# Optimization experiments

Hardware: AMD Instinct MI355X
Metric: run time of the kernel (lower is better)

The kernel has to match this reference:

```python
import jax, jax.numpy as jnp
import numpy as np

B, T, C = 4, 2048, 1024   # batch, seq_len, n_embd
H, D = 16, 64             # num heads, head dim (H*D == C)


def setup_inputs() -> dict:
    key = jax.random.key(0)
    ks = jax.random.split(key, 6)
    scale = 0.02
    x = jax.random.normal(ks[0], (B, T, C), dtype=jnp.float32)
    Wq = jax.random.normal(ks[1], (H, C, D), dtype=jnp.float32) * scale
    Wk = jax.random.normal(ks[2], (H, C, D), dtype=jnp.float32) * scale
    Wv = jax.random.normal(ks[3], (H, C, D), dtype=jnp.float32) * scale
    Wp = jax.random.normal(ks[4], (C, C), dtype=jnp.float32) * scale
    bp = jnp.zeros((C,), dtype=jnp.float32)
    return {"x": x, "Wq": Wq, "Wk": Wk, "Wv": Wv, "Wp": Wp, "bp": bp}


def reference(x, Wq, Wk, Wv, Wp, bp):
    # Batched per-head projections (equivalent to the per-head nn.Linear loop)
    q = jnp.einsum('btc,hcd->bhtd', x, Wq)
    k = jnp.einsum('btc,hcd->bhtd', x, Wk)
    v = jnp.einsum('btc,hcd->bhtd', x, Wv)
    # NOTE: original code scales by C**-0.5 where C = n_embd (not head dim)
    scores = jnp.einsum('bhtd,bhsd->bhts', q, k) * (C ** -0.5)
    causal = jnp.tril(jnp.ones((T, T), dtype=bool))  # [T, T]
    scores = jnp.where(causal, scores, -jnp.inf)
    att = jax.nn.softmax(scores, axis=-1)            # [B, H, T, T]
    out = jnp.einsum('bhts,bhsd->bhtd', att, v)      # [B, H, T, D]
    # concat heads (order matches torch.cat over head list) then output proj
    out = out.transpose(0, 2, 1, 3).reshape(B, T, H * D)
    return out @ Wp + bp
```

## Files before the change

### kernel.cpp

```cpp
#include <hip/hip_runtime.h>
#include <hip/hip_bf16.h>


#define B_ 4
#define T_ 2048
#define C_ 1024
#define H_ 16
#define D_ 64
#define M_ (B_*T_)

typedef unsigned short u16;
typedef unsigned short ushort8 __attribute__((ext_vector_type(8)));
typedef unsigned int uint4v __attribute__((ext_vector_type(4)));
typedef int int2v __attribute__((ext_vector_type(2)));
typedef __attribute__((ext_vector_type(8))) short bf16x8;
typedef __attribute__((ext_vector_type(4))) float f32x4;
typedef __attribute__((ext_vector_type(16))) float f32x16;

__device__ __forceinline__ u16 f2bf(float f) {
    __hip_bfloat16 h = __float2bfloat16(f);
    return *reinterpret_cast<u16*>(&h);
}

__device__ __forceinline__ unsigned pkt(float lo, float hi2) {
    return __builtin_amdgcn_perm(__float_as_uint(hi2), __float_as_uint(lo), 0x07060302u);
}

__device__ __forceinline__ void gload_lds16(const void* g, void* lds) {
    __builtin_amdgcn_global_load_lds((const __attribute__((address_space(1))) unsigned int*)g,
                                     (__attribute__((address_space(3))) unsigned int*)lds, 16, 0, 0);
}

__global__ __launch_bounds__(256) void cast_x(const float* __restrict__ in, u16* __restrict__ out) {
    int i = (blockIdx.x * 256 + threadIdx.x) * 8;
    float4 a = *reinterpret_cast<const float4*>(in + i);
    float4 b = *reinterpret_cast<const float4*>(in + i + 4);
    ushort8 o;
    o[0]=f2bf(a.x); o[1]=f2bf(a.y); o[2]=f2bf(a.z); o[3]=f2bf(a.w);
    o[4]=f2bf(b.x); o[5]=f2bf(b.y); o[6]=f2bf(b.z); o[7]=f2bf(b.w);
    *reinterpret_cast<ushort8*>(out + i) = o;
}

__device__ __forceinline__ void ttile64(const float* __restrict__ in, int ldin,
                                        u16* __restrict__ out, int ldout, float scale) {
    __shared__ float t[64][65];
    const int tid = threadIdx.x;
    {
        int c = tid & 63, rr = tid >> 6;
        #pragma unroll
        for (int i = 0; i < 16; ++i) {
            int r = i * 4 + rr;
            t[r][c] = in[(size_t)r * ldin + c];
        }
    }
    __syncthreads();
    {
        int r2 = tid & 63, cg = tid >> 6;
        #pragma unroll
        for (int i = 0; i < 16; ++i) {
            int cc = i * 4 + cg;
            out[(size_t)cc * ldout + r2] = f2bf(t[r2][cc] * scale);
        }
    }
}

__global__ __launch_bounds__(256) void tw_qkv(const float* __restrict__ Wq, const float* __restrict__ Wk,
                                              const float* __restrict__ Wv, u16* __restrict__ Wt) {
    const int z = blockIdx.y;
    const int which = z >> 4, h = z & 15;
    const float* W = (which == 0 ? Wq : which == 1 ? Wk : Wv) + (size_t)h * C_ * D_;
    const int r0 = blockIdx.x * 64;
    const float scale = (which == 0) ? 0.03125f * 1.4426950408889634f : 1.f;
    ttile64(W + (size_t)r0 * D_, D_, Wt + (size_t)(which * 16 + h) * 64 * C_ + r0, C_, scale);
}

__global__ __launch_bounds__(256) void tw_p(const float* __restrict__ Wp, u16* __restrict__ Wpt) {
    const int r0 = blockIdx.x * 64, c0 = blockIdx.y * 64;
    ttile64(Wp + (size_t)r0 * C_ + c0, C_, Wpt + (size_t)c0 * C_ + r0, C_, 1.f);
}

__global__ __launch_bounds__(256) void tv(const u16* __restrict__ v, u16* __restrict__ vT) {
    __shared__ u16 t[64][72];
    const int tid = threadIdx.x;
    const int t0 = blockIdx.x * 64, bh = blockIdx.y;
    const u16* src = v + ((size_t)bh * T_ + t0) * D_;
    #pragma unroll
    for (int it = 0; it < 2; ++it) {
        int idx = it * 256 + tid;
        int r = idx >> 3, c8 = (idx & 7) * 8;
        *reinterpret_cast<ushort8*>(&t[r][c8]) =
            *reinterpret_cast<const ushort8*>(src + (size_t)r * D_ + c8);
    }
    __syncthreads();
    #pragma unroll
    for (int it = 0; it < 2; ++it) {
        int idx = it * 256 + tid;
        int d = idx >> 3, c8 = (idx & 7) * 8;
        ushort8 w;
        #pragma unroll
        for (int i = 0; i < 8; ++i) w[i] = t[c8 + i][d];
        *reinterpret_cast<ushort8*>(vT + ((size_t)bh * D_ + d) * T_ + t0 + c8) = w;
    }
}

__device__ __forceinline__ void gemm128_core(const u16* __restrict__ A, const u16* __restrict__ Bt,
                                             int m0, int n0, int K,
                                             u16* Asm, u16* Bsm, f32x4 (&acc)[4][4]) {
    const int tid = threadIdx.x;
    const int wid = tid >> 6, lane = tid & 63;
    const int l16 = lane & 15, lq = lane >> 4;
    const int wm = wid >> 1, wn = wid & 1;
    const int srow = lane >> 2;
    const int scol = (lane & 3) * 8;

    for (int k0 = 0; k0 < K; k0 += 32) {
        __syncthreads();
        #pragma unroll
        for (int it = 0; it < 2; ++it) {
            int row = wid * 32 + it * 16 + srow;
            gload_lds16(A  + (size_t)(m0 + row) * K + k0 + scol, Asm + wid * 1024 + it * 512);
            gload_lds16(Bt + (size_t)(n0 + row) * K + k0 + scol, Bsm + wid * 1024 + it * 512);
        }
        __syncthreads();
        bf16x8 af[4], bfr[4];
        #pragma unroll
        for (int t = 0; t < 4; ++t) {
            af[t]  = *reinterpret_cast<const bf16x8*>(Asm + (wm * 64 + t * 16 + l16) * 32 + lq * 8);
            bfr[t] = *reinterpret_cast<const bf16x8*>(Bsm + (wn * 64 + t * 16 + l16) * 32 + lq * 8);
        }
        #pragma unroll
        for (int mt = 0; mt < 4; ++mt)
            #pragma unroll
            for (int nt = 0; nt < 4; ++nt)
                acc[mt][nt] = __builtin_amdgcn_mfma_f32_16x16x32_bf16(af[mt], bfr[nt], acc[mt][nt], 0, 0, 0);
    }
}

__global__ __launch_bounds__(256) void qkv_gemm(const u16* __restrict__ xb, const u16* __restrict__ Wt,
                                                u16* __restrict__ q, u16* __restrict__ k, u16* __restrict__ v) {
    __shared__ u16 Asm[128 * 32], Bsm[128 * 32];
    f32x4 acc[4][4];
    #pragma unroll
    for (int i = 0; i < 4; ++i)
        #pragma unroll
        for (int j = 0; j < 4; ++j) { acc[i][j][0]=0.f; acc[i][j][1]=0.f; acc[i][j][2]=0.f; acc[i][j][3]=0.f; }
    const int m0 = blockIdx.x * 128, n0 = blockIdx.y * 128;
    gemm128_core(xb, Wt, m0, n0, C_, Asm, Bsm, acc);

    const int tid = threadIdx.x, wid = tid >> 6, lane = tid & 63;
    const int l16 = lane & 15, lq = lane >> 4;
    const int wm = wid >> 1, wn = wid & 1;
    #pragma unroll
    for (int mt = 0; mt < 4; ++mt) {
        #pragma unroll
        for (int j = 0; j < 4; ++j) {
            int m = m0 + wm * 64 + mt * 16 + lq * 4 + j;
            int b = m >> 11, t = m & (T_ - 1);
            #pragma unroll
            for (int nt = 0; nt < 4; ++nt) {
                int n = n0 + wn * 64 + nt * 16 + l16;
                int which = n >> 10, h = (n >> 6) & 15, d = n & 63;
                u16* dst = (which == 0 ? q : which == 1 ? k : v);
                dst[((size_t)(b * H_ + h) * T_ + t) * D_ + d] = f2bf(acc[mt][nt][j]);
            }
        }
    }
}

__global__ __launch_bounds__(256) void out_gemm(const u16* __restrict__ ob, const u16* __restrict__ Wpt,
                                                const float* __restrict__ bp, float* __restrict__ out) {
    __shared__ u16 Asm[128 * 32], Bsm[128 * 32];
    f32x4 acc[4][4];
    #pragma unroll
    for (int i = 0; i < 4; ++i)
        #pragma unroll
        for (int j = 0; j < 4; ++j) { acc[i][j][0]=0.f; acc[i][j][1]=0.f; acc[i][j][2]=0.f; acc[i][j][3]=0.f; }
    const int m0 = blockIdx.x * 128, n0 = blockIdx.y * 128;
    gemm128_core(ob, Wpt, m0, n0, C_, Asm, Bsm, acc);

    const int tid = threadIdx.x, wid = tid >> 6, lane = tid & 63;
    const int l16 = lane & 15, lq = lane >> 4;
    const int wm = wid >> 1, wn = wid & 1;
    #pragma unroll
    for (int mt = 0; mt < 4; ++mt) {
        #pragma unroll
        for (int j = 0; j < 4; ++j) {
            int m = m0 + wm * 64 + mt * 16 + lq * 4 + j;
            #pragma unroll
            for (int nt = 0; nt < 4; ++nt) {
                int n = n0 + wn * 64 + nt * 16 + l16;
                out[(size_t)m * C_ + n] = acc[mt][nt][j] + bp[n];
            }
        }
    }
}

template<int CUR>
__device__ __forceinline__ void attn_tile(const char* const (&pf)[4], const bf16x8 (&qf)[4],
                                          const f32x16& z16, float& lrun,
                                          f32x16& oacc0, f32x16& oacc1,
                                          bool isdiag, int relq, int hi) {
    f32x16 st0, st1;
    __builtin_amdgcn_s_setprio(1);
    {
        bf16x8 ka0 = *reinterpret_cast<const bf16x8*>(pf[0] + CUR * 8192);
        bf16x8 ka1 = *reinterpret_cast<const bf16x8*>(pf[0] + CUR * 8192 + 4096);
        st0 = __builtin_amdgcn_mfma_f32_32x32x16_bf16(ka0, qf[0], z16, 0, 0, 0);
        st1 = __builtin_amdgcn_mfma_f32_32x32x16_bf16(ka1, qf[0], z16, 0, 0, 0);
    }
    #pragma unroll
    for (int kc = 1; kc < 4; ++kc) {
        bf16x8 ka0 = *reinterpret_cast<const bf16x8*>(pf[kc] + CUR * 8192);
        bf16x8 ka1 = *reinterpret_cast<const bf16x8*>(pf[kc] + CUR * 8192 + 4096);
        st0 = __builtin_amdgcn_mfma_f32_32x32x16_bf16(ka0, qf[kc], st0, 0, 0, 0);
        st1 = __builtin_amdgcn_mfma_f32_32x32x16_bf16(ka1, qf[kc], st1, 0, 0, 0);
    }
    __builtin_amdgcn_s_setprio(0);

    if (isdiag) {
        #pragma unroll
        for (int rr = 0; rr < 16; ++rr) {
            int sl = (rr & 3) + 8 * (rr >> 2) + 4 * hi;
            if (sl > relq)      st0[rr] = -INFINITY;
            if (sl + 32 > relq) st1[rr] = -INFINITY;
        }
    }

    float rsum = 0.f;
    #pragma unroll
    for (int rr = 0; rr < 16; ++rr) {
        st0[rr] = __builtin_amdgcn_exp2f(st0[rr]);
        st1[rr] = __builtin_amdgcn_exp2f(st1[rr]);
        rsum += st0[rr] + st1[rr];
    }
    rsum += __shfl_xor(rsum, 32);
    lrun += rsum;

    bf16x8 pa0, pa1, pa2, pa3;
#if __has_builtin(__builtin_amdgcn_permlane32_swap)
#define MK_PA(PA, SV, RB)                                                          \
    {                                                                              \
        int X0 = (int)pkt(SV[RB + 0], SV[RB + 1]);                                 \
        int X1 = (int)pkt(SV[RB + 2], SV[RB + 3]);                                 \
        int Y0 = (int)pkt(SV[RB + 4], SV[RB + 5]);                                 \
        int Y1 = (int)pkt(SV[RB + 6], SV[RB + 7]);                                 \
        int2v r0 = __builtin_amdgcn_permlane32_swap(X0, Y0, false, false);         \
        int2v r1 = __builtin_amdgcn_permlane32_swap(X1, Y1, false, false);         \
        uint4v w; w[0] = (unsigned)r0[0]; w[1] = (unsigned)r1[0];                  \
        w[2] = (unsigned)r0[1]; w[3] = (unsigned)r1[1];                            \
        PA = __builtin_bit_cast(bf16x8, w);                                        \
    }
#else
#define MK_PA(PA, SV, RB)                                                          \
    {                                                                              \
        unsigned X0 = pkt(SV[RB + 0], SV[RB + 1]);                                 \
        unsigned X1 = pkt(SV[RB + 2], SV[RB + 3]);                                 \
        unsigned Y0 = pkt(SV[RB + 4], SV[RB + 5]);                                 \
        unsigned sX0 = __shfl_xor(X0, 32), sY0 = __shfl_xor(Y0, 32);               \
        unsigned Y1 = pkt(SV[RB + 6], SV[RB + 7]);                                 \
        unsigned sX1 = __shfl_xor(X1, 32), sY1 = __shfl_xor(Y1, 32);               \
        uint4v w;                                                                  \
        w[0] = hi ? sY0 : X0; w[1] = hi ? sY1 : X1;                                \
        w[2] = hi ? Y0 : sX0; w[3] = hi ? Y1 : sX1;                                \
        PA = __builtin_bit_cast(bf16x8, w);                                        \
    }
#endif
    MK_PA(pa0, st0, 0); MK_PA(pa1, st0, 8); MK_PA(pa2, st1, 0); MK_PA(pa3, st1, 8);
#undef MK_PA

    __builtin_amdgcn_s_setprio(1);
#define PV_STEP(SCJ, PAV)                                                          \
    {                                                                              \
        bf16x8 va0 = *reinterpret_cast<const bf16x8*>(pf[SCJ] + 16384 + CUR * 8192);        \
        bf16x8 va1 = *reinterpret_cast<const bf16x8*>(pf[SCJ] + 16384 + CUR * 8192 + 4096); \
        oacc0 = __builtin_amdgcn_mfma_f32_32x32x16_bf16(va0, PAV, oacc0, 0, 0, 0); \
        oacc1 = __builtin_amdgcn_mfma_f32_32x32x16_bf16(va1, PAV, oacc1, 0, 0, 0); \
    }
    PV_STEP(0, pa0) PV_STEP(1, pa1) PV_STEP(2, pa2) PV_STEP(3, pa3)
#undef PV_STEP
    __builtin_amdgcn_s_setprio(0);
}

__global__ __launch_bounds__(256) void attn_mfma(const u16* __restrict__ q,
                                                 const u16* __restrict__ k,
                                                 const u16* __restrict__ vT,
                                                 u16* __restrict__ o) {
    __shared__ u16 smem[2][2][4096];

    const int tid  = threadIdx.x;
    const int wid  = tid >> 6;
    const int lane = tid & 63;
    const int l31  = lane & 31;
    const int hi   = lane >> 5;

    const int lin = blockIdx.x;
    const int r   = lin & 255;
    const int f   = lin >> 8;
    const int e   = r & 7;
    int qb, bh;
    if      (f == 0) { qb = e;      bh = (r >> 3);      }
    else if (f == 1) { qb = 15 - e; bh = (r >> 3);      }
    else if (f == 2) { qb = e + 8;  bh = (r >> 3) + 32; }
    else             { qb = 7 - e;  bh = (r >> 3) + 32; }

    const int q0 = qb * 128;
    const size_t base = (size_t)bh * T_ * D_;
    const u16* kp  = k  + base;
    const u16* vtp = vT + (size_t)bh * D_ * T_;
    const int qglob = q0 + wid * 32 + l31;

    bf16x8 qf[4];
    {
        const u16* qp = q + base + (size_t)qglob * D_;
        #pragma unroll
        for (int kc = 0; kc < 4; ++kc)
            qf[kc] = *reinterpret_cast<const bf16x8*>(qp + kc * 16 + hi * 8);
    }

    const int rw0 = wid * 8 + (lane >> 3);
    const int rw1 = rw0 + 32;
    const int cg  = (lane & 7) ^ (rw0 & 7);
    const u16* gK0 = kp + rw0 * D_ + cg * 8;
    const u16* gK1 = kp + rw1 * D_ + cg * 8;
    const u16* gV0 = vtp + (size_t)rw0 * T_ + cg * 8;
    const u16* gV1 = vtp + (size_t)rw1 * T_ + cg * 8;

    u16* sbase = &smem[0][0][0];
    u16* dK0 = sbase + wid * 512;
    u16* dK1 = sbase + 2048 + wid * 512;
    u16* dV0 = sbase + 8192 + wid * 512;
    u16* dV1 = sbase + 8192 + 2048 + wid * 512;

    const char* pf[4];
    #pragma unroll
    for (int j = 0; j < 4; ++j)
        pf[j] = reinterpret_cast<const char*>(sbase) + l31 * 128 + (((j * 2 + hi) ^ (l31 & 7)) << 4);

    float lrun = 0.f;
    f32x16 oacc0, oacc1, z16;
    #pragma unroll
    for (int rr = 0; rr < 16; ++rr) { oacc0[rr] = 0.f; oacc1[rr] = 0.f; z16[rr] = 0.f; }

    const int ntile  = 2 * qb + 2;
    const int diag_t = 2 * qb + (wid >> 1);
    const int relq   = 32 * (wid & 1) + l31;

#define STG(BUFOFF)                                                                \
    {                                                                              \
        gload_lds16(gK0, dK0 + (BUFOFF)); gload_lds16(gK1, dK1 + (BUFOFF));        \
        gload_lds16(gV0, dV0 + (BUFOFF)); gload_lds16(gV1, dV1 + (BUFOFF));        \
        gK0 += 64 * D_; gK1 += 64 * D_; gV0 += 64; gV1 += 64;                      \
    }

    STG(0);
    __syncthreads();

    for (int tt = 0; tt < ntile; tt += 2) {
        if (tt + 1 < ntile) STG(4096);
        if (tt <= diag_t)
            attn_tile<0>(pf, qf, z16, lrun, oacc0, oacc1, tt == diag_t, relq, hi);
        __syncthreads();
        if (tt + 2 < ntile) STG(0);
        if (tt + 1 <= diag_t)
            attn_tile<1>(pf, qf, z16, lrun, oacc0, oacc1, tt + 1 == diag_t, relq, hi);
        __syncthreads();
    }
#undef STG

    float linv = 1.f / lrun;
    float* ot = reinterpret_cast<float*>(sbase) + wid * 2048;
    #pragma unroll
    for (int rr = 0; rr < 16; ++rr) {
        int d0v = (rr & 3) + 8 * (rr >> 2) + 4 * hi;
        int d1v = d0v + 32;
        ot[l31 * 64 + (((d0v >> 2) ^ (l31 & 7)) << 2) + (d0v & 3)] = oacc0[rr] * linv;
        ot[l31 * 64 + (((d1v >> 2) ^ (l31 & 7)) << 2) + (d1v & 3)] = oacc1[rr] * linv;
    }

    const int b = bh >> 4, h = bh & 15;
    const int qrow = lane >> 1;
    const int d0 = (lane & 1) * 32;
    u16 tmp[32];
    #pragma unroll
    for (int i = 0; i < 8; ++i) {
        int g = ((d0 >> 2) + i) ^ (qrow & 7);
        float4 fv = *reinterpret_cast<const float4*>(&ot[qrow * 64 + (g << 2)]);
        tmp[i * 4 + 0] = f2bf(fv.x); tmp[i * 4 + 1] = f2bf(fv.y);
        tmp[i * 4 + 2] = f2bf(fv.z); tmp[i * 4 + 3] = f2bf(fv.w);
    }
    u16* orow = o + ((size_t)b * T_ + q0 + wid * 32 + qrow) * C_ + h * 64 + d0;
    #pragma unroll
    for (int j = 0; j < 4; ++j)
        *reinterpret_cast<ushort8*>(orow + j * 8) = *reinterpret_cast<ushort8*>(&tmp[j * 8]);
}

extern "C" void kernel_launch(void* const* d_in, const int* in_sizes, int n_in,
                              void* d_out, int out_size, void* d_ws, size_t ws_size,
                              hipStream_t stream) {
    const float* x  = (const float*)d_in[0];
    const float* Wq = (const float*)d_in[1];
    const float* Wk = (const float*)d_in[2];
    const float* Wv = (const float*)d_in[3];
    const float* Wp = (const float*)d_in[4];
    const float* bp = (const float*)d_in[5];
    float* out = (float*)d_out;

    const size_t E = (size_t)M_ * C_;
    u16* xb  = (u16*)d_ws;
    u16* qb  = xb  + E;
    u16* kb  = qb  + E;
    u16* vb  = kb  + E;
    u16* obf = vb  + E;
    u16* Wt  = obf + E;
    u16* Wpt = Wt  + (size_t)3072 * 1024;
    u16* vTb = xb;

    cast_x<<<(E / 2048), 256, 0, stream>>>(x, xb);
    tw_qkv<<<dim3(16, 48), 256, 0, stream>>>(Wq, Wk, Wv, Wt);
    tw_p<<<dim3(16, 16), 256, 0, stream>>>(Wp, Wpt);

    qkv_gemm<<<dim3(M_ / 128, 3072 / 128), 256, 0, stream>>>(xb, Wt, qb, kb, vb);

    tv<<<dim3(T_ / 64, B_ * H_), 256, 0, stream>>>(vb, vTb);

    attn_mfma<<<dim3(1024), 256, 0, stream>>>(qb, kb, vTb, obf);

    out_gemm<<<dim3(M_ / 128, C_ / 128), 256, 0, stream>>>(obf, Wpt, bp, out);
}
```

Measured before the change: 165.4 us.

## Rewrite projection GEMMs with 256x128 tiles, triple-buffered LDS and swizzle

Replaces the 128x128, K=32 single-buffered GEMM core with a 256x128 tile, 512-thread kernel that uses K=64 stages in a three-deep LDS ring buffer with explicit vmcnt waits, so global-to-LDS loads overlap MFMA work. LDS rows are XOR-swizzled to avoid bank conflicts, and each wave computes a 128x32 sub-tile. The aim is to remove load stalls and per-step barrier overhead in the QKV and output projections. In exchange it uses much more LDS per block (144KB) and more registers, which limits occupancy and halves the number of blocks.

```diff
diff --git a/kernel.cpp b/kernel.cpp
--- a/kernel.cpp
+++ b/kernel.cpp
@@ -103,62 +103,108 @@
     }
 }
 
-__device__ __forceinline__ void gemm128_core(const u16* __restrict__ A, const u16* __restrict__ Bt,
-                                             int m0, int n0, int K,
-                                             u16* Asm, u16* Bsm, f32x4 (&acc)[4][4]) {
+__device__ __forceinline__ void gemm256_core(const u16* __restrict__ A, const u16* __restrict__ Bt,
+                                             int m0, int n0, u16* lds, f32x4 (&acc)[8][2]) {
     const int tid = threadIdx.x;
     const int wid = tid >> 6, lane = tid & 63;
     const int l16 = lane & 15, lq = lane >> 4;
-    const int wm = wid >> 1, wn = wid & 1;
-    const int srow = lane >> 2;
-    const int scol = (lane & 3) * 8;
-
-    for (int k0 = 0; k0 < K; k0 += 32) {
-        __syncthreads();
-        #pragma unroll
-        for (int it = 0; it < 2; ++it) {
-            int row = wid * 32 + it * 16 + srow;
-            gload_lds16(A  + (size_t)(m0 + row) * K + k0 + scol, Asm + wid * 1024 + it * 512);
-            gload_lds16(Bt + (size_t)(n0 + row) * K + k0 + scol, Bsm + wid * 1024 + it * 512);
-        }
-        __syncthreads();
-        bf16x8 af[4], bfr[4];
-        #pragma unroll
-        for (int t = 0; t < 4; ++t) {
-            af[t]  = *reinterpret_cast<const bf16x8*>(Asm + (wm * 64 + t * 16 + l16) * 32 + lq * 8);
-            bfr[t] = *reinterpret_cast<const bf16x8*>(Bsm + (wn * 64 + t * 16 + l16) * 32 + lq * 8);
-        }
-        #pragma unroll
-        for (int mt = 0; mt < 4; ++mt)
+    const int wr = wid >> 2, wc = wid & 3;
+
+    const u16* sA[4];
+    const u16* sB[2];
+    #pragma unroll
+    for (int it = 0; it < 4; ++it) {
+        int slot = it * 512 + tid, row = slot >> 3, gd = slot & 7;
+        sA[it] = A + (size_t)(m0 + row) * C_ + ((gd ^ (row & 7)) * 8);
+    }
+    #pragma unroll
+    for (int it = 0; it < 2; ++it) {
+        int slot = it * 512 + tid, row = slot >> 3, gd = slot & 7;
+        sB[it] = Bt + (size_t)(n0 + row) * C_ + ((gd ^ (row & 7)) * 8);
+    }
+    const int dA = wid * 512 + lane * 8;
+    const int dB = 16384 + wid * 512 + lane * 8;
+
+    const char* lb = reinterpret_cast<const char*>(lds);
+    const int arow = wr * 128 + l16;
+    const int brow = wc * 32 + l16;
+    const int g0 = (lq ^ (l16 & 7)) * 16;
+    const int g1 = ((4 + lq) ^ (l16 & 7)) * 16;
+    const int aoff0 = arow * 128 + g0, aoff1 = arow * 128 + g1;
+    const int boff0 = 32768 + brow * 128 + g0, boff1 = 32768 + brow * 128 + g1;
+
+#define STAGE6(BUFU16)                                                              \
+    {                                                                               \
+        _Pragma("unroll")                                                           \
+        for (int it = 0; it < 4; ++it) {                                            \
+            gload_lds16(sA[it], lds + (BUFU16) + it * 4096 + dA);                   \
+            sA[it] += 64;                                                           \
+        }                                                                           \
+        _Pragma("unroll")                                                           \
+        for (int it = 0; it < 2; ++it) {                                            \
+            gload_lds16(sB[it], lds + (BUFU16) + it * 4096 + dB);                   \
+            sB[it] += 64;                                                           \
+        }                                                                           \
+    }
+
+    STAGE6(0);
+    STAGE6(24576);
+
+    #pragma unroll
+    for (int t = 0; t < 16; ++t) {
+        if (t + 2 < 16) STAGE6(((t + 2) % 3) * 24576);
+        if (t + 2 < 16)      { asm volatile("s_waitcnt vmcnt(12)" ::: "memory"); }
+        else if (t + 1 < 16) { asm volatile("s_waitcnt vmcnt(6)" ::: "memory"); }
+        else                 { asm volatile("s_waitcnt vmcnt(0)" ::: "memory"); }
+        __builtin_amdgcn_sched_barrier(0);
+        __builtin_amdgcn_s_barrier();
+        __builtin_amdgcn_sched_barrier(0);
+
+        const char* lbuf = lb + (size_t)((t % 3) * 24576) * 2;
+        __builtin_amdgcn_s_setprio(1);
+        #pragma unroll
+        for (int kc = 0; kc < 2; ++kc) {
+            bf16x8 bf0 = *reinterpret_cast<const bf16x8*>(lbuf + (kc ? boff1 : boff0));
+            bf16x8 bf1 = *reinterpret_cast<const bf16x8*>(lbuf + (kc ? boff1 : boff0) + 2048);
             #pragma unroll
-            for (int nt = 0; nt < 4; ++nt)
-                acc[mt][nt] = __builtin_amdgcn_mfma_f32_16x16x32_bf16(af[mt], bfr[nt], acc[mt][nt], 0, 0, 0);
-    }
-}
-
-__global__ __launch_bounds__(256) void qkv_gemm(const u16* __restrict__ xb, const u16* __restrict__ Wt,
-                                                u16* __restrict__ q, u16* __restrict__ k, u16* __restrict__ v) {
-    __shared__ u16 Asm[128 * 32], Bsm[128 * 32];
-    f32x4 acc[4][4];
-    #pragma unroll
-    for (int i = 0; i < 4; ++i)
-        #pragma unroll
-        for (int j = 0; j < 4; ++j) { acc[i][j][0]=0.f; acc[i][j][1]=0.f; acc[i][j][2]=0.f; acc[i][j][3]=0.f; }
-    const int m0 = blockIdx.x * 128, n0 = blockIdx.y * 128;
-    gemm128_core(xb, Wt, m0, n0, C_, Asm, Bsm, acc);
+            for (int mt = 0; mt < 8; ++mt) {
+                bf16x8 af = *reinterpret_cast<const bf16x8*>(lbuf + (kc ? aoff1 : aoff0) + mt * 2048);
+                acc[mt][0] = __builtin_amdgcn_mfma_f32_16x16x32_bf16(af, bf0, acc[mt][0], 0, 0, 0);
+                acc[mt][1] = __builtin_amdgcn_mfma_f32_16x16x32_bf16(af, bf1, acc[mt][1], 0, 0, 0);
+            }
+        }
+        __builtin_amdgcn_s_setprio(0);
+        __builtin_amdgcn_sched_barrier(0);
+        __builtin_amdgcn_s_barrier();
+        __builtin_amdgcn_sched_barrier(0);
+    }
+#undef STAGE6
+}
+
+__global__ __launch_bounds__(512, 2) void qkv_gemm(const u16* __restrict__ xb, const u16* __restrict__ Wt,
+                                                   u16* __restrict__ q, u16* __restrict__ k,
+                                                   u16* __restrict__ v) {
+    __shared__ u16 lds[3 * 24576];
+    f32x4 acc[8][2];
+    #pragma unroll
+    for (int i = 0; i < 8; ++i)
+        #pragma unroll
+        for (int j = 0; j < 2; ++j) { acc[i][j][0]=0.f; acc[i][j][1]=0.f; acc[i][j][2]=0.f; acc[i][j][3]=0.f; }
+    const int m0 = blockIdx.x * 256, n0 = blockIdx.y * 128;
+    gemm256_core(xb, Wt, m0, n0, lds, acc);
 
     const int tid = threadIdx.x, wid = tid >> 6, lane = tid & 63;
     const int l16 = lane & 15, lq = lane >> 4;
-    const int wm = wid >> 1, wn = wid & 1;
-    #pragma unroll
-    for (int mt = 0; mt < 4; ++mt) {
+    const int wr = wid >> 2, wc = wid & 3;
+    #pragma unroll
+    for (int mt = 0; mt < 8; ++mt) {
         #pragma unroll
         for (int j = 0; j < 4; ++j) {
-            int m = m0 + wm * 64 + mt * 16 + lq * 4 + j;
+            int m = m0 + wr * 128 + mt * 16 + lq * 4 + j;
             int b = m >> 11, t = m & (T_ - 1);
             #pragma unroll
-            for (int nt = 0; nt < 4; ++nt) {
-                int n = n0 + wn * 64 + nt * 16 + l16;
+            for (int nt = 0; nt < 2; ++nt) {
+                int n = n0 + wc * 32 + nt * 16 + l16;
                 int which = n >> 10, h = (n >> 6) & 15, d = n & 63;
                 u16* dst = (which == 0 ? q : which == 1 ? k : v);
                 dst[((size_t)(b * H_ + h) * T_ + t) * D_ + d] = f2bf(acc[mt][nt][j]);
@@ -167,28 +213,28 @@
     }
 }
 
-__global__ __launch_bounds__(256) void out_gemm(const u16* __restrict__ ob, const u16* __restrict__ Wpt,
-                                                const float* __restrict__ bp, float* __restrict__ out) {
-    __shared__ u16 Asm[128 * 32], Bsm[128 * 32];
-    f32x4 acc[4][4];
-    #pragma unroll
-    for (int i = 0; i < 4; ++i)
-        #pragma unroll
-        for (int j = 0; j < 4; ++j) { acc[i][j][0]=0.f; acc[i][j][1]=0.f; acc[i][j][2]=0.f; acc[i][j][3]=0.f; }
-    const int m0 = blockIdx.x * 128, n0 = blockIdx.y * 128;
-    gemm128_core(ob, Wpt, m0, n0, C_, Asm, Bsm, acc);
+__global__ __launch_bounds__(512, 2) void out_gemm(const u16* __restrict__ ob, const u16* __restrict__ Wpt,
+                                                   const float* __restrict__ bp, float* __restrict__ out) {
+    __shared__ u16 lds[3 * 24576];
+    f32x4 acc[8][2];
+    #pragma unroll
+    for (int i = 0; i < 8; ++i)
+        #pragma unroll
+        for (int j = 0; j < 2; ++j) { acc[i][j][0]=0.f; acc[i][j][1]=0.f; acc[i][j][2]=0.f; acc[i][j][3]=0.f; }
+    const int m0 = blockIdx.x * 256, n0 = blockIdx.y * 128;
+    gemm256_core(ob, Wpt, m0, n0, lds, acc);
 
     const int tid = threadIdx.x, wid = tid >> 6, lane = tid & 63;
     const int l16 = lane & 15, lq = lane >> 4;
-    const int wm = wid >> 1, wn = wid & 1;
-    #pragma unroll
-    for (int mt = 0; mt < 4; ++mt) {
+    const int wr = wid >> 2, wc = wid & 3;
+    #pragma unroll
+    for (int mt = 0; mt < 8; ++mt) {
         #pragma unroll
         for (int j = 0; j < 4; ++j) {
-            int m = m0 + wm * 64 + mt * 16 + lq * 4 + j;
+            int m = m0 + wr * 128 + mt * 16 + lq * 4 + j;
             #pragma unroll
-            for (int nt = 0; nt < 4; ++nt) {
-                int n = n0 + wn * 64 + nt * 16 + l16;
+            for (int nt = 0; nt < 2; ++nt) {
+                int n = n0 + wc * 32 + nt * 16 + l16;
                 out[(size_t)m * C_ + n] = acc[mt][nt][j] + bp[n];
             }
         }
@@ -419,11 +465,11 @@
     tw_qkv<<<dim3(16, 48), 256, 0, stream>>>(Wq, Wk, Wv, Wt);
     tw_p<<<dim3(16, 16), 256, 0, stream>>>(Wp, Wpt);
 
-    qkv_gemm<<<dim3(M_ / 128, 3072 / 128), 256, 0, stream>>>(xb, Wt, qb, kb, vb);
+    qkv_gemm<<<dim3(M_ / 256, 3072 / 128), 512, 0, stream>>>(xb, Wt, qb, kb, vb);
 
     tv<<<dim3(T_ / 64, B_ * H_), 256, 0, stream>>>(vb, vTb);
 
     attn_mfma<<<dim3(1024), 256, 0, stream>>>(qb, kb, vTb, obf);
 
-    out_gemm<<<dim3(M_ / 128, C_ / 128), 256, 0, stream>>>(obf, Wpt, bp, out);
-}
+    out_gemm<<<dim3(M_ / 256, C_ / 128), 512, 0, stream>>>(obf, Wpt, bp, out);
+}
```

New measurement: 156.2 us. 1.06x faster.
